# Kernel tuning notes

Hardware: AMD Instinct MI355X
Metric: run time of the kernel (lower is better)

Reference implementation:

```python
import jax, jax.numpy as jnp
import numpy as np

N = 50000          # num nodes
E = 800000         # num edges
DIM = 64           # node_channels
EDGE_DIM = 16
HEADS = 4
TIME_STEP = 3
NEG_SLOPE = 0.2
HC = HEADS * DIM


def setup_inputs() -> dict:
    key = jax.random.key(0)
    ks = jax.random.split(key, 16)
    rn = lambda k, shape, s=0.1: (jax.random.normal(k, shape, jnp.float32) * s)
    return {
        "x": jax.random.normal(ks[0], (N, DIM), jnp.float32),
        "edge_index": jax.random.randint(ks[1], (2, E), 0, N, jnp.int32),
        "edge_attr": jax.random.normal(ks[2], (E, EDGE_DIM), jnp.float32),
        "Wn": rn(ks[3], (DIM, HC)),
        "We": rn(ks[4], (EDGE_DIM, HC)),
        "Wa": rn(ks[5], (1, HEADS, 3 * DIM)),
        "Ws": rn(ks[6], (HC, DIM)),
        "b": jnp.zeros((DIM,), jnp.float32),
        "Wih": rn(ks[7], (3 * DIM, DIM)),
        "Whh": rn(ks[8], (3 * DIM, DIM)),
        "bih": rn(ks[9], (3 * DIM,)),
        "bhh": rn(ks[10], (3 * DIM,)),
        "gamma": jnp.ones((DIM,), jnp.float32),
        "beta": jnp.zeros((DIM,), jnp.float32),
    }


def _mhta(x, src, dst, edge_attr, Wn, We, Wa, Ws, b):
    xp = x @ Wn                                    # [N, H*C]
    ep = (edge_attr @ We).reshape(-1, HEADS, DIM)  # [E, H, C]
    x_j = xp[src].reshape(-1, HEADS, DIM)          # source nodes
    x_i = xp[dst].reshape(-1, HEADS, DIM)          # target nodes
    wa = Wa.reshape(HEADS, 3, DIM)                 # split of cat([x_i, e, x_j])
    alpha = (jnp.einsum('ehc,hc->eh', x_i, wa[:, 0])
             + jnp.einsum('ehc,hc->eh', ep, wa[:, 1])
             + jnp.einsum('ehc,hc->eh', x_j, wa[:, 2]))
    alpha = jax.nn.leaky_relu(alpha, NEG_SLOPE)
    # segment softmax grouped by target node (PyG softmax)
    amax = jax.ops.segment_max(alpha, dst, num_segments=N)
    alpha = jnp.exp(alpha - amax[dst])
    denom = jax.ops.segment_sum(alpha, dst, num_segments=N)
    alpha = alpha / (denom[dst] + 1e-16)
    msg = (alpha[:, :, None] * ep * x_j).reshape(-1, HC)
    aggr = jax.ops.segment_sum(msg, dst, num_segments=N)  # [N, H*C]
    return aggr @ Ws + b


def _gru_step(m, h, Wih, Whh, bih, bhh):
    gi = m @ Wih.T + bih
    gh = h @ Whh.T + bhh
    i_r, i_z, i_n = jnp.split(gi, 3, axis=-1)
    h_r, h_z, h_n = jnp.split(gh, 3, axis=-1)
    r = jax.nn.sigmoid(i_r + h_r)
    z = jax.nn.sigmoid(i_z + h_z)
    n = jnp.tanh(i_n + r * h_n)
    return (1.0 - z) * n + z * h


def _layernorm(x, gamma, beta, eps=1e-5):
    mu = jnp.mean(x, axis=-1, keepdims=True)
    var = jnp.mean((x - mu) ** 2, axis=-1, keepdims=True)
    return (x - mu) * jax.lax.rsqrt(var + eps) * gamma + beta


def reference(x, edge_index, edge_attr, Wn, We, Wa, Ws, b,
              Wih, Whh, bih, bhh, gamma, beta):
    src, dst = edge_index[0], edge_index[1]
    h = x  # h0 = x.unsqueeze(0) in torch (seq_len=1 GRU)
    xc = x
    for _ in range(TIME_STEP):
        m = jax.nn.celu(_mhta(xc, src, dst, edge_attr, Wn, We, Wa, Ws, b))
        h = _gru_step(m, h, Wih, Whh, bih, bhh)
        xc = _layernorm(h, gamma, beta)
    return xc
```

## Files before the change

### kernel.cpp

```cpp
#include <hip/hip_runtime.h>
#include <math.h>

#define NNODES 50000
#define NEDGES 800000

typedef _Float16 f16;
typedef _Float16 f16x2 __attribute__((ext_vector_type(2)));
typedef _Float16 f16x4 __attribute__((ext_vector_type(4)));
typedef _Float16 f16x8 __attribute__((ext_vector_type(8)));
typedef float f32x4 __attribute__((ext_vector_type(4)));

#define FMAMIX_LO(ACC, PV, WRD) \
    asm("v_fma_mix_f32 %0, %1, %2, %0 op_sel_hi:[0,1,0]" \
        : "+v"(ACC) : "v"(PV), "v"(WRD))
#define FMAMIX_HI(ACC, PV, WRD) \
    asm("v_fma_mix_f32 %0, %1, %2, %0 op_sel:[0,1,0] op_sel_hi:[0,1,0]" \
        : "+v"(ACC) : "v"(PV), "v"(WRD))

__device__ inline uint pk16(float a, float b) {
    union { f16x2 h; uint u; } c;
    c.h[0] = (f16)a; c.h[1] = (f16)b;
    return c.u;
}
__device__ inline f16x2 bc16(uint u) {
    union { uint u; f16x2 h; } c; c.u = u; return c.h;
}
__device__ inline float wred_max(float v) {
#pragma unroll
    for (int off = 32; off; off >>= 1) v = fmaxf(v, __shfl_xor(v, off, 64));
    return v;
}
__device__ inline float wred_sum(float v) {
#pragma unroll
    for (int off = 32; off; off >>= 1) v += __shfl_xor(v, off, 64);
    return v;
}
__device__ inline float wred_max16(float v) {
#pragma unroll
    for (int off = 8; off; off >>= 1) v = fmaxf(v, __shfl_xor(v, off, 64));
    return v;
}
__device__ inline float wred_sum16(float v) {
#pragma unroll
    for (int off = 8; off; off >>= 1) v += __shfl_xor(v, off, 64);
    return v;
}


__global__ __launch_bounds__(256) void k_fold1(
    const float* __restrict__ Wn, const float* __restrict__ We,
    const float* __restrict__ Wa,
    float* __restrict__ wnwa0, float* __restrict__ wnwa2,
    float* __restrict__ wewa1)
{
    int t = threadIdx.x;
    {
        int k = t >> 2, h = t & 3;
        float s0 = 0.f, s2 = 0.f;
        for (int c = 0; c < 64; c++) {
            float wn = Wn[k * 256 + h * 64 + c];
            s0 = fmaf(wn, Wa[h * 192 + c], s0);
            s2 = fmaf(wn, Wa[h * 192 + 128 + c], s2);
        }
        wnwa0[t] = s0;
        wnwa2[t] = s2;
    }
    if (t < 64) {
        int k = t >> 2, h = t & 3;
        float s1 = 0.f;
        for (int c = 0; c < 64; c++)
            s1 = fmaf(We[k * 256 + h * 64 + c], Wa[h * 192 + 64 + c], s1);
        wewa1[t] = s1;
    }
}

__global__ __launch_bounds__(256) void k_fold2(
    const float* __restrict__ Wn, const float* __restrict__ We,
    const float* __restrict__ Wih, const float* __restrict__ Whh,
    const float* __restrict__ Ws, const float* __restrict__ wnwa0,
    const float* __restrict__ wnwa2,
    f16* __restrict__ WeB, f16* __restrict__ WsP, f16* __restrict__ WihP,
    f16* __restrict__ WhhP, f16* __restrict__ WnB, f16* __restrict__ awB)
{
    int gid = blockIdx.x * 256 + threadIdx.x;
    const int STR = 8 * 256;
    for (int idx = gid; idx < 128; idx += STR) {
        int ks = idx >> 6, l = idx & 63;
        int lg = l >> 4, c = l & 15;
        f16* o = awB + (size_t)idx * 8;
        for (int j = 0; j < 8; j++) {
            int k = ks * 32 + lg * 8 + j;
            float v = (c < 4) ? wnwa0[k * 4 + c] : ((c < 8) ? wnwa2[k * 4 + (c - 4)] : 0.f);
            o[j] = (f16)v;
        }
    }
    for (int idx = gid; idx < 2048; idx += STR) {
        int l = idx & 63, tt = (idx >> 6) & 15, ks = idx >> 10;
        int lg = l >> 4, ll = l & 15;
        f16* o = WnB + (size_t)idx * 8;
        for (int j = 0; j < 8; j++)
            o[j] = (f16)Wn[(ks * 32 + lg * 8 + j) * 256 + tt * 16 + ll];
    }
    for (int idx = gid; idx < 1024; idx += STR) {
        int tt = idx >> 6, l = idx & 63;
        int lg = l >> 4, ll = l & 15;
        f16* o = WeB + (size_t)idx * 4;
        for (int j = 0; j < 4; j++)
            o[j] = (f16)We[(lg * 4 + j) * 256 + tt * 16 + ll];
    }
    for (int e = gid; e < 2048; e += STR) {
        int l = e & 63, tt = (e >> 6) & 3, ks = e >> 8;
        int lg = l >> 4, ll = l & 15;
        f16* o = WsP + (size_t)e * 8;
        for (int j = 0; j < 8; j++)
            o[j] = (f16)Ws[(ks * 32 + lg * 8 + j) * 64 + tt * 16 + ll];
    }
    for (int e = gid; e < 1536; e += STR) {
        int l = e & 63, q = e >> 6;
        int tt = q % 12, ks = q / 12;
        int lg = l >> 4, ll = l & 15;
        int outc = tt * 16 + ll;
        for (int j = 0; j < 8; j++) {
            int k = ks * 32 + lg * 8 + j;
            WihP[(size_t)e * 8 + j] = (f16)Wih[outc * 64 + k];
            WhhP[(size_t)e * 8 + j] = (f16)Whh[outc * 64 + k];
        }
    }
}

__global__ __launch_bounds__(256) void k_hist(const int* __restrict__ dst, int* __restrict__ counts)
{
    int e = blockIdx.x * 256 + threadIdx.x;
    atomicAdd(&counts[dst[e]], 1);
}

__global__ __launch_bounds__(1024) void k_scan(const int* __restrict__ counts,
                                               int* __restrict__ row_ptr, int n)
{
    __shared__ int wsum[16];
    int t = threadIdx.x, wid = t >> 6, lane = t & 63;
    int running = 0;
    for (int base = 0; base < n; base += 1024) {
        int idx = base + t;
        int c = (idx < n) ? counts[idx] : 0;
        int v = c;
#pragma unroll
        for (int off = 1; off < 64; off <<= 1) {
            int u = __shfl_up(v, off, 64);
            if (lane >= off) v += u;
        }
        if (lane == 63) wsum[wid] = v;
        __syncthreads();
        int wpre = 0, tot = 0;
#pragma unroll
        for (int wk = 0; wk < 16; wk++) {
            int s = wsum[wk];
            if (wk < wid) wpre += s;
            tot += s;
        }
        if (idx < n) row_ptr[idx] = running + wpre + v - c;
        running += tot;
        __syncthreads();
    }
    if (t == 0) row_ptr[n] = running;
}

__global__ __launch_bounds__(256) void k_scatter(
    const int* __restrict__ srcv, const int* __restrict__ dstv,
    const float* __restrict__ ea, const float* __restrict__ wewa1,
    const int* __restrict__ row_ptr, int* __restrict__ fill,
    int* __restrict__ csr_src, uint* __restrict__ ae16c,
    uint* __restrict__ ea16_csr)
{
    __shared__ float w[64];
    int t = threadIdx.x;
    if (t < 64) w[t] = wewa1[t];
    __syncthreads();
    int e = blockIdx.x * 256 + t;
    int d = dstv[e];
    int pos = row_ptr[d] + atomicAdd(&fill[d], 1);
    csr_src[pos] = srcv[e];
    const float4* p = (const float4*)(ea + (size_t)e * 16);
    float4 v0 = p[0], v1 = p[1], v2 = p[2], v3 = p[3];
    float eav[16] = {v0.x, v0.y, v0.z, v0.w, v1.x, v1.y, v1.z, v1.w,
                     v2.x, v2.y, v2.z, v2.w, v3.x, v3.y, v3.z, v3.w};
    float a0 = 0.f, a1 = 0.f, a2 = 0.f, a3 = 0.f;
#pragma unroll
    for (int k = 0; k < 16; k++) {
        a0 = fmaf(eav[k], w[k * 4 + 0], a0);
        a1 = fmaf(eav[k], w[k * 4 + 1], a1);
        a2 = fmaf(eav[k], w[k * 4 + 2], a2);
        a3 = fmaf(eav[k], w[k * 4 + 3], a3);
    }
    uint2 ae2; ae2.x = pk16(a0, a1); ae2.y = pk16(a2, a3);
    *(uint2*)(ae16c + (size_t)pos * 2) = ae2;
    uint4 pa, pb;
    pa.x = pk16(eav[0], eav[1]);  pa.y = pk16(eav[2], eav[3]);
    pa.z = pk16(eav[4], eav[5]);  pa.w = pk16(eav[6], eav[7]);
    pb.x = pk16(eav[8], eav[9]);  pb.y = pk16(eav[10], eav[11]);
    pb.z = pk16(eav[12], eav[13]); pb.w = pk16(eav[14], eav[15]);
    uint4* d16 = (uint4*)(ea16_csr + (size_t)pos * 8);
    d16[0] = pa; d16[1] = pb;
}


__global__ __launch_bounds__(256) void k_xpaij(
    const float* __restrict__ xc, const f16* __restrict__ WnB,
    const f16* __restrict__ awB, f16* __restrict__ xp16,
    float* __restrict__ aijI, float* __restrict__ aijJ)
{
    int t = threadIdx.x, w = t >> 6, l = t & 63;
    int lg = l >> 4, ll = l & 15;
    int wbase = blockIdx.x * 64 + w * 16;
    int nodeA = wbase + ll;
    int nA = nodeA < NNODES ? nodeA : NNODES - 1;

    f16x8 afr[2];
#pragma unroll
    for (int ks = 0; ks < 2; ks++) {
        const float* xpr = xc + (size_t)nA * 64 + ks * 32 + lg * 8;
        float4 a0 = *(const float4*)xpr;
        float4 a1 = *(const float4*)(xpr + 4);
        f16x8 v;
        v[0] = (f16)a0.x; v[1] = (f16)a0.y; v[2] = (f16)a0.z; v[3] = (f16)a0.w;
        v[4] = (f16)a1.x; v[5] = (f16)a1.y; v[6] = (f16)a1.z; v[7] = (f16)a1.w;
        afr[ks] = v;
    }
    f32x4 zero = {0.f, 0.f, 0.f, 0.f};
    f32x4 c[16];
#pragma unroll
    for (int tt = 0; tt < 16; tt++) c[tt] = zero;
    f32x4 caw = zero;
    const f16x8* WnV = (const f16x8*)WnB;
    const f16x8* awV = (const f16x8*)awB;
#pragma unroll
    for (int ks = 0; ks < 2; ks++) {
        caw = __builtin_amdgcn_mfma_f32_16x16x32_f16(afr[ks], awV[ks * 64 + l], caw, 0, 0, 0);
#pragma unroll
        for (int tt = 0; tt < 16; tt++)
            c[tt] = __builtin_amdgcn_mfma_f32_16x16x32_f16(
                afr[ks], WnV[(ks * 16 + tt) * 64 + l], c[tt], 0, 0, 0);
    }
#pragma unroll
    for (int i = 0; i < 4; i++) {
        int node = wbase + lg * 4 + i;
        if (node < NNODES) {
            f16x8 o0, o1;
#pragma unroll
            for (int tt = 0; tt < 8; tt++) o0[tt] = (f16)c[tt][i];
#pragma unroll
            for (int tt = 0; tt < 8; tt++) o1[tt] = (f16)c[8 + tt][i];
            f16* dstp = xp16 + (size_t)node * 256 + ll * 16;
            *(f16x8*)dstp = o0;
            *(f16x8*)(dstp + 8) = o1;
            if (ll < 4)      aijI[(size_t)node * 4 + ll] = caw[i];
            else if (ll < 8) aijJ[(size_t)node * 4 + (ll - 4)] = caw[i];
        }
    }
}

#define LEAKY(v) ((v) > 0.f ? (v) : 0.2f * (v))

__global__ __launch_bounds__(256) void k_node(
    const int* __restrict__ row_ptr, const int* __restrict__ csr_src,
    const uint* __restrict__ ae16c, const float* __restrict__ aijI,
    const float* __restrict__ aijJ, const f16* __restrict__ xp16,
    const uint* __restrict__ ea16_csr, const f16* __restrict__ WeB,
    f16* __restrict__ aggr16)
{
    __shared__ float wbuf[4][64][4];
    __shared__ uint  eabuf[4][64][8];
    __shared__ int   srcbuf[4][64];
    int t = threadIdx.x, wid = t >> 6, lane = t & 63;
    int ll = lane & 15, g = lane >> 4;
    int n = blockIdx.x * 4 + wid;
    uint4 z4 = {0u, 0u, 0u, 0u};
    *(uint4*)&eabuf[wid][lane][0] = z4;
    *(uint4*)&eabuf[wid][lane][4] = z4;
    f16x4 wb[16];
#pragma unroll
    for (int tt = 0; tt < 16; tt++)
        wb[tt] = *(const f16x4*)(WeB + (size_t)(tt * 64 + lane) * 4);
    int r0 = row_ptr[n], r1 = row_ptr[n + 1];
    int deg = r1 - r0;
    float acc[16];
#pragma unroll
    for (int tt = 0; tt < 16; tt++) acc[tt] = 0.f;
    f32x4 zacc = {0.f, 0.f, 0.f, 0.f};

    auto agg_chunk = [&](int c) {
        int4 s4 = *(const int4*)&srcbuf[wid][c * 16 + g * 4];
        const f16* xr0 = xp16 + ((size_t)(uint)s4.x) * 256 + ll * 16;
        const f16* xr1 = xp16 + ((size_t)(uint)s4.y) * 256 + ll * 16;
        const f16* xr2 = xp16 + ((size_t)(uint)s4.z) * 256 + ll * 16;
        const f16* xr3 = xp16 + ((size_t)(uint)s4.w) * 256 + ll * 16;
        uint4 xA[4], xB[4];
        xA[0] = *(const uint4*)xr0; xB[0] = *(const uint4*)(xr0 + 8);
        xA[1] = *(const uint4*)xr1; xB[1] = *(const uint4*)(xr1 + 8);
        xA[2] = *(const uint4*)xr2; xB[2] = *(const uint4*)(xr2 + 8);
        xA[3] = *(const uint4*)xr3; xB[3] = *(const uint4*)(xr3 + 8);
        f16x4 eaf = *(const f16x4*)((const f16*)&eabuf[wid][c * 16 + ll][0] + g * 4);
        float4 w4 = *(const float4*)&wbuf[wid][c * 16 + ll][0];
        f16 av[4] = {(f16)w4.x, (f16)w4.y, (f16)w4.z, (f16)w4.w};
        f16x4 Ah[4];
#pragma unroll
        for (int h = 0; h < 4; h++)
#pragma unroll
            for (int j = 0; j < 4; j++)
                Ah[h][j] = eaf[j] * av[h];
#pragma unroll
        for (int h = 0; h < 4; h++) {
            f32x4 p0 = __builtin_amdgcn_mfma_f32_16x16x16f16(Ah[h], wb[h * 4 + 0], zacc, 0, 0, 0);
            f32x4 p1 = __builtin_amdgcn_mfma_f32_16x16x16f16(Ah[h], wb[h * 4 + 1], zacc, 0, 0, 0);
            f32x4 p2 = __builtin_amdgcn_mfma_f32_16x16x16f16(Ah[h], wb[h * 4 + 2], zacc, 0, 0, 0);
            f32x4 p3 = __builtin_amdgcn_mfma_f32_16x16x16f16(Ah[h], wb[h * 4 + 3], zacc, 0, 0, 0);
#pragma unroll
            for (int ttl = 0; ttl < 4; ttl++) {
                int tt = h * 4 + ttl;
                f32x4 pv = ttl == 0 ? p0 : (ttl == 1 ? p1 : (ttl == 2 ? p2 : p3));
                int q = tt & 7;
#pragma unroll
                for (int r = 0; r < 4; r++) {
                    uint4 xs = (tt < 8) ? xA[r] : xB[r];
                    uint wrd = (q >> 1) == 0 ? xs.x
                             : ((q >> 1) == 1 ? xs.y : ((q >> 1) == 2 ? xs.z : xs.w));
                    float pvf = pv[r];
                    if (q & 1) FMAMIX_HI(acc[tt], pvf, wrd);
                    else       FMAMIX_LO(acc[tt], pvf, wrd);
                }
            }
        }
    };

    if (deg > 0 && deg <= 64) {
        float4 ai = *(const float4*)(aijI + (size_t)n * 4);
        float al0 = -1e30f, al1 = -1e30f, al2 = -1e30f, al3 = -1e30f;
        int sreg = 0;
        if (lane < deg) {
            int p = r0 + lane;
            sreg = csr_src[p];
            uint2 ae2 = *(const uint2*)(ae16c + (size_t)p * 2);
            f16x2 aelo = bc16(ae2.x), aehi = bc16(ae2.y);
            float4 aj = *(const float4*)(aijJ + (size_t)sreg * 4);
            const uint4* ep16 = (const uint4*)(ea16_csr + (size_t)p * 8);
            uint4 ua = ep16[0], ub = ep16[1];
            *(uint4*)&eabuf[wid][lane][0] = ua;
            *(uint4*)&eabuf[wid][lane][4] = ub;
            al0 = LEAKY(ai.x + (float)aelo[0] + aj.x);
            al1 = LEAKY(ai.y + (float)aelo[1] + aj.y);
            al2 = LEAKY(ai.z + (float)aehi[0] + aj.z);
            al3 = LEAKY(ai.w + (float)aehi[1] + aj.w);
        }
        srcbuf[wid][lane] = (lane < deg) ? sreg : 0;
        float m0, m1, m2, m3, s0, s1, s2, s3;
        float p0, p1, p2, p3;
        if (deg <= 16) {
            m0 = wred_max16(al0); m1 = wred_max16(al1);
            m2 = wred_max16(al2); m3 = wred_max16(al3);
            p0 = (lane < deg) ? __expf(al0 - m0) : 0.f;
            p1 = (lane < deg) ? __expf(al1 - m1) : 0.f;
            p2 = (lane < deg) ? __expf(al2 - m2) : 0.f;
            p3 = (lane < deg) ? __expf(al3 - m3) : 0.f;
            s0 = wred_sum16(p0); s1 = wred_sum16(p1);
            s2 = wred_sum16(p2); s3 = wred_sum16(p3);
        } else {
            m0 = wred_max(al0); m1 = wred_max(al1);
            m2 = wred_max(al2); m3 = wred_max(al3);
            p0 = (lane < deg) ? __expf(al0 - m0) : 0.f;
            p1 = (lane < deg) ? __expf(al1 - m1) : 0.f;
            p2 = (lane < deg) ? __expf(al2 - m2) : 0.f;
            p3 = (lane < deg) ? __expf(al3 - m3) : 0.f;
            s0 = wred_sum(p0); s1 = wred_sum(p1);
            s2 = wred_sum(p2); s3 = wred_sum(p3);
        }
        float4 w4v;
        w4v.x = p0 * (1.f / (s0 + 1e-16f));
        w4v.y = p1 * (1.f / (s1 + 1e-16f));
        w4v.z = p2 * (1.f / (s2 + 1e-16f));
        w4v.w = p3 * (1.f / (s3 + 1e-16f));
        *(float4*)&wbuf[wid][lane][0] = w4v;
        asm volatile("s_waitcnt lgkmcnt(0)" ::: "memory");
        int nch = (deg + 15) >> 4;
        for (int c = 0; c < nch; c++) agg_chunk(c);
    } else if (deg > 0) {
        float4 ai = *(const float4*)(aijI + (size_t)n * 4);
        float m0 = -1e30f, m1 = -1e30f, m2 = -1e30f, m3 = -1e30f;
        float s0 = 0.f, s1 = 0.f, s2 = 0.f, s3 = 0.f;
        for (int base = r0; base < r1; base += 64) {
            int p = base + lane;
            if (p < r1) {
                int s = csr_src[p];
                uint2 ae2 = *(const uint2*)(ae16c + (size_t)p * 2);
                f16x2 aelo = bc16(ae2.x), aehi = bc16(ae2.y);
                float4 aj = *(const float4*)(aijJ + (size_t)s * 4);
                float al0 = LEAKY(ai.x + (float)aelo[0] + aj.x);
                float al1 = LEAKY(ai.y + (float)aelo[1] + aj.y);
                float al2 = LEAKY(ai.z + (float)aehi[0] + aj.z);
                float al3 = LEAKY(ai.w + (float)aehi[1] + aj.w);
                float nm;
                nm = fmaxf(m0, al0); s0 = s0 * __expf(m0 - nm) + __expf(al0 - nm); m0 = nm;
                nm = fmaxf(m1, al1); s1 = s1 * __expf(m1 - nm) + __expf(al1 - nm); m1 = nm;
                nm = fmaxf(m2, al2); s2 = s2 * __expf(m2 - nm) + __expf(al2 - nm); m2 = nm;
                nm = fmaxf(m3, al3); s3 = s3 * __expf(m3 - nm) + __expf(al3 - nm); m3 = nm;
            }
        }
#pragma unroll
        for (int off = 32; off; off >>= 1) {
            float om, os, nm;
            om = __shfl_xor(m0, off, 64); os = __shfl_xor(s0, off, 64);
            nm = fmaxf(m0, om); s0 = s0 * __expf(m0 - nm) + os * __expf(om - nm); m0 = nm;
            om = __shfl_xor(m1, off, 64); os = __shfl_xor(s1, off, 64);
            nm = fmaxf(m1, om); s1 = s1 * __expf(m1 - nm) + os * __expf(om - nm); m1 = nm;
            om = __shfl_xor(m2, off, 64); os = __shfl_xor(s2, off, 64);
            nm = fmaxf(m2, om); s2 = s2 * __expf(m2 - nm) + os * __expf(om - nm); m2 = nm;
            om = __shfl_xor(m3, off, 64); os = __shfl_xor(s3, off, 64);
            nm = fmaxf(m3, om); s3 = s3 * __expf(m3 - nm) + os * __expf(om - nm); m3 = nm;
        }
        float rd0 = 1.f / (s0 + 1e-16f), rd1 = 1.f / (s1 + 1e-16f);
        float rd2 = 1.f / (s2 + 1e-16f), rd3 = 1.f / (s3 + 1e-16f);
        for (int base = r0; base < r1; base += 64) {
            int cnt = min(64, r1 - base);
            float4 w4v = {0.f, 0.f, 0.f, 0.f};
            int sreg = 0;
            if (lane < cnt) {
                int p = base + lane;
                sreg = csr_src[p];
                uint2 ae2 = *(const uint2*)(ae16c + (size_t)p * 2);
                f16x2 aelo = bc16(ae2.x), aehi = bc16(ae2.y);
                float4 aj = *(const float4*)(aijJ + (size_t)sreg * 4);
                const uint4* ep16 = (const uint4*)(ea16_csr + (size_t)p * 8);
                uint4 ua = ep16[0], ub = ep16[1];
                *(uint4*)&eabuf[wid][lane][0] = ua;
                *(uint4*)&eabuf[wid][lane][4] = ub;
                float al0 = LEAKY(ai.x + (float)aelo[0] + aj.x);
                float al1 = LEAKY(ai.y + (float)aelo[1] + aj.y);
                float al2 = LEAKY(ai.z + (float)aehi[0] + aj.z);
                float al3 = LEAKY(ai.w + (float)aehi[1] + aj.w);
                w4v.x = __expf(al0 - m0) * rd0;
                w4v.y = __expf(al1 - m1) * rd1;
                w4v.z = __expf(al2 - m2) * rd2;
                w4v.w = __expf(al3 - m3) * rd3;
            } else {
                *(uint4*)&eabuf[wid][lane][0] = z4;
                *(uint4*)&eabuf[wid][lane][4] = z4;
            }
            *(float4*)&wbuf[wid][lane][0] = w4v;
            srcbuf[wid][lane] = (lane < cnt) ? sreg : 0;
            asm volatile("s_waitcnt lgkmcnt(0)" ::: "memory");
            int nch = (cnt + 15) >> 4;
            for (int c = 0; c < nch; c++) agg_chunk(c);
            asm volatile("s_waitcnt lgkmcnt(0)" ::: "memory");
        }
    }
#pragma unroll
    for (int tt = 0; tt < 16; tt++) {
        float v = acc[tt];
        v += __shfl_xor(v, 16, 64);
        v += __shfl_xor(v, 32, 64);
        acc[tt] = v;
    }
    f16* ag = aggr16 + (size_t)n * 256;
#pragma unroll
    for (int tt = 0; tt < 16; tt++)
        if ((tt >> 2) == g) ag[tt * 16 + ll] = (f16)acc[tt];
}

__global__ __launch_bounds__(256) void k_post(
    const f16* __restrict__ aggr16, const f16* __restrict__ WsP,
    const float* __restrict__ bvec, const float* __restrict__ h_in,
    float* __restrict__ h_out, const f16* __restrict__ WihP,
    const f16* __restrict__ WhhP, const float* __restrict__ bih,
    const float* __restrict__ bhh, const float* __restrict__ gamma,
    const float* __restrict__ beta, float* __restrict__ xc_out)
{
    __shared__ __align__(16) f16 m_lds[4][16][72];
    int t = threadIdx.x, w = t >> 6, l = t & 63;
    int lg = l >> 4, ll = l & 15;
    int nb = blockIdx.x * 64 + w * 16;
    int nodeA = nb + ll;
    int nodeAc = nodeA < NNODES ? nodeA : NNODES - 1;

    f32x4 zero = {0.f, 0.f, 0.f, 0.f};
    f32x4 acc1[4];
#pragma unroll
    for (int tt = 0; tt < 4; tt++) acc1[tt] = zero;
    const f16x8* WsV = (const f16x8*)WsP;
#pragma unroll
    for (int ks = 0; ks < 8; ks++) {
        f16x8 a = *(const f16x8*)(aggr16 + (size_t)nodeAc * 256 + ks * 32 + lg * 8);
#pragma unroll
        for (int tt = 0; tt < 4; tt++) {
            f16x8 b = WsV[(ks * 4 + tt) * 64 + l];
            acc1[tt] = __builtin_amdgcn_mfma_f32_16x16x32_f16(a, b, acc1[tt], 0, 0, 0);
        }
    }
#pragma unroll
    for (int tt = 0; tt < 4; tt++) {
        float bj = bvec[tt * 16 + ll];
#pragma unroll
        for (int i = 0; i < 4; i++) {
            float v = acc1[tt][i] + bj;
            v = v > 0.f ? v : (__expf(v) - 1.f);
            m_lds[w][lg * 4 + i][tt * 16 + ll] = (f16)v;
        }
    }
    asm volatile("s_waitcnt lgkmcnt(0)" ::: "memory");

    f16x8 mf[2], hf[2];
#pragma unroll
    for (int ks = 0; ks < 2; ks++) {
        mf[ks] = *(const f16x8*)(&m_lds[w][ll][ks * 32 + lg * 8]);
        const float* hp = h_in + (size_t)nodeAc * 64 + ks * 32 + lg * 8;
        float4 h0 = *(const float4*)(hp);
        float4 h1 = *(const float4*)(hp + 4);
        f16x8 hh;
        hh[0] = (f16)h0.x; hh[1] = (f16)h0.y; hh[2] = (f16)h0.z; hh[3] = (f16)h0.w;
        hh[4] = (f16)h1.x; hh[5] = (f16)h1.y; hh[6] = (f16)h1.z; hh[7] = (f16)h1.w;
        hf[ks] = hh;
    }
    f32x4 accI[12], accH[12];
#pragma unroll
    for (int tt = 0; tt < 12; tt++) { accI[tt] = zero; accH[tt] = zero; }
    const f16x8* WiV = (const f16x8*)WihP;
    const f16x8* WhV = (const f16x8*)WhhP;
#pragma unroll
    for (int ks = 0; ks < 2; ks++) {
#pragma unroll
        for (int tt = 0; tt < 12; tt++) {
            f16x8 bi = WiV[(ks * 12 + tt) * 64 + l];
            accI[tt] = __builtin_amdgcn_mfma_f32_16x16x32_f16(mf[ks], bi, accI[tt], 0, 0, 0);
            f16x8 bh = WhV[(ks * 12 + tt) * 64 + l];
            accH[tt] = __builtin_amdgcn_mfma_f32_16x16x32_f16(hf[ks], bh, accH[tt], 0, 0, 0);
        }
    }

    float bI[12], bH[12];
#pragma unroll
    for (int tt = 0; tt < 12; tt++) {
        bI[tt] = bih[ll + 16 * tt];
        bH[tt] = bhh[ll + 16 * tt];
    }
    float ga[4], be[4];
#pragma unroll
    for (int u = 0; u < 4; u++) { ga[u] = gamma[ll + 16 * u]; be[u] = beta[ll + 16 * u]; }
    float hnew[4][4];
#pragma unroll
    for (int i = 0; i < 4; i++) {
        int node = nb + lg * 4 + i;
        int nc = node < NNODES ? node : NNODES - 1;
        const float* hrow = h_in + (size_t)nc * 64 + ll;
#pragma unroll
        for (int u = 0; u < 4; u++) {
            float hv = hrow[16 * u];
            float r = 1.f / (1.f + __expf(-(accI[u][i] + bI[u] + accH[u][i] + bH[u])));
            float z = 1.f / (1.f + __expf(-(accI[u + 4][i] + bI[u + 4] + accH[u + 4][i] + bH[u + 4])));
            float pre = accI[u + 8][i] + bI[u + 8] + r * (accH[u + 8][i] + bH[u + 8]);
            float e2 = __expf(2.f * pre);
            float nn = 1.f - 2.f / (e2 + 1.f);
            hnew[i][u] = (1.f - z) * nn + z * hv;
        }
    }
#pragma unroll
    for (int i = 0; i < 4; i++) {
        float s = hnew[i][0] + hnew[i][1] + hnew[i][2] + hnew[i][3];
        float q = hnew[i][0] * hnew[i][0] + hnew[i][1] * hnew[i][1]
                + hnew[i][2] * hnew[i][2] + hnew[i][3] * hnew[i][3];
#pragma unroll
        for (int off = 1; off < 16; off <<= 1) {
            s += __shfl_xor(s, off, 64);
            q += __shfl_xor(q, off, 64);
        }
        float mu = s * (1.f / 64.f);
        float var = q * (1.f / 64.f) - mu * mu;
        float rstd = rsqrtf(var + 1e-5f);
        int node = nb + lg * 4 + i;
        if (node < NNODES) {
            float* ho = h_out + (size_t)node * 64 + ll;
            float* xo = xc_out + (size_t)node * 64 + ll;
#pragma unroll
            for (int u = 0; u < 4; u++) {
                ho[16 * u] = hnew[i][u];
                xo[16 * u] = (hnew[i][u] - mu) * rstd * ga[u] + be[u];
            }
        }
    }
}


extern "C" void kernel_launch(void* const* d_in, const int* in_sizes, int n_in,
                              void* d_out, int out_size, void* d_ws, size_t ws_size,
                              hipStream_t stream)
{
    const float* x         = (const float*)d_in[0];
    const int*   edge_index= (const int*)d_in[1];
    const float* edge_attr = (const float*)d_in[2];
    const float* Wn        = (const float*)d_in[3];
    const float* We        = (const float*)d_in[4];
    const float* Wa        = (const float*)d_in[5];
    const float* Ws        = (const float*)d_in[6];
    const float* bv        = (const float*)d_in[7];
    const float* Wih       = (const float*)d_in[8];
    const float* Whh       = (const float*)d_in[9];
    const float* bih       = (const float*)d_in[10];
    const float* bhh       = (const float*)d_in[11];
    const float* gamma     = (const float*)d_in[12];
    const float* beta      = (const float*)d_in[13];
    float* out = (float*)d_out;

    const int* src = edge_index;
    const int* dst = edge_index + NEDGES;

    char* w = (char*)d_ws;
    auto alloc = [&](size_t bytes) {
        char* p = w;
        w += (bytes + 255) & ~(size_t)255;
        return p;
    };
    f16*   xp16     = (f16*)alloc((size_t)NNODES * 256 * 2);
    f16*   aggr16   = (f16*)alloc((size_t)NNODES * 256 * 2);
    uint*  ae16c    = (uint*)alloc((size_t)NEDGES * 2 * 4);
    uint*  ea16_csr = (uint*)alloc((size_t)NEDGES * 8 * 4);
    float* hbuf     = (float*)alloc((size_t)NNODES * 64 * 4);
    float* aijI     = (float*)alloc((size_t)NNODES * 4 * 4);
    float* aijJ     = (float*)alloc((size_t)NNODES * 4 * 4);
    int*   counts   = (int*)alloc((size_t)NNODES * 4);
    int*   fill     = (int*)alloc((size_t)NNODES * 4);
    int*   row_ptr  = (int*)alloc((size_t)(NNODES + 1) * 4);
    int*   csr_src  = (int*)alloc((size_t)NEDGES * 4);
    float* wnwa0    = (float*)alloc(256 * 4);
    float* wnwa2    = (float*)alloc(256 * 4);
    float* wewa1    = (float*)alloc(64 * 4);
    f16*   WeB      = (f16*)alloc(1024 * 4 * 2);
    f16*   WsP      = (f16*)alloc(2048 * 8 * 2);
    f16*   WihP     = (f16*)alloc(1536 * 8 * 2);
    f16*   WhhP     = (f16*)alloc(1536 * 8 * 2);
    f16*   WnB      = (f16*)alloc(2048 * 8 * 2);
    f16*   awB      = (f16*)alloc(128 * 8 * 2);

    k_fold1<<<1, 256, 0, stream>>>(Wn, We, Wa, wnwa0, wnwa2, wewa1);
    hipMemsetAsync(counts, 0, (size_t)NNODES * 4, stream);
    hipMemsetAsync(fill, 0, (size_t)NNODES * 4, stream);
    k_hist<<<NEDGES / 256, 256, 0, stream>>>(dst, counts);
    k_fold2<<<8, 256, 0, stream>>>(Wn, We, Wih, Whh, Ws, wnwa0, wnwa2,
                                   WeB, WsP, WihP, WhhP, WnB, awB);
    k_scan<<<1, 1024, 0, stream>>>(counts, row_ptr, NNODES);
    k_scatter<<<NEDGES / 256, 256, 0, stream>>>(src, dst, edge_attr, wewa1,
                                                row_ptr, fill, csr_src,
                                                ae16c, ea16_csr);

    for (int step = 0; step < 3; step++) {
        const float* xc_in = (step == 0) ? x : out;
        const float* h_in  = (step == 0) ? x : hbuf;
        k_xpaij<<<(NNODES + 63) / 64, 256, 0, stream>>>(xc_in, WnB, awB,
                                                        xp16, aijI, aijJ);
        k_node<<<NNODES / 4, 256, 0, stream>>>(row_ptr, csr_src, ae16c, aijI,
                                               aijJ, xp16, ea16_csr, WeB, aggr16);
        k_post<<<(NNODES + 63) / 64, 256, 0, stream>>>(
            aggr16, WsP, bv, h_in, hbuf, WihP, WhhP, bih, bhh, gamma, beta, out);
    }
}
```

Baseline: 575.6 us.

## Fuse next-step node projection into GRU post kernel and parallelize CSR scan

Replaces the single-block serial scan with a three-pass multi-block scan. k_hist now records each edge's atomic rank, so k_scatter no longer needs a second atomic fill pass. The k_xpaij projection for steps 1 and 2 is folded into k_post: the layernormed output goes through LDS as f16 and is multiplied by Wn and the attention weights with MFMA, which removes the intermediate xc write and read and two kernel launches. The costs are an extra per-edge rank buffer and higher register pressure in k_post.

```diff
diff --git a/kernel.cpp b/kernel.cpp
--- a/kernel.cpp
+++ b/kernel.cpp
@@ -128,47 +128,72 @@
     }
 }
 
-__global__ __launch_bounds__(256) void k_hist(const int* __restrict__ dst, int* __restrict__ counts)
+__global__ __launch_bounds__(256) void k_hist(const int* __restrict__ dst,
+                                              int* __restrict__ counts,
+                                              int* __restrict__ rankv)
 {
     int e = blockIdx.x * 256 + threadIdx.x;
-    atomicAdd(&counts[dst[e]], 1);
-}
-
-__global__ __launch_bounds__(1024) void k_scan(const int* __restrict__ counts,
-                                               int* __restrict__ row_ptr, int n)
+    rankv[e] = atomicAdd(&counts[dst[e]], 1);
+}
+
+__global__ __launch_bounds__(1024) void k_scan1(const int* __restrict__ counts,
+                                                int* __restrict__ psum)
 {
     __shared__ int wsum[16];
     int t = threadIdx.x, wid = t >> 6, lane = t & 63;
-    int running = 0;
-    for (int base = 0; base < n; base += 1024) {
-        int idx = base + t;
-        int c = (idx < n) ? counts[idx] : 0;
-        int v = c;
-#pragma unroll
-        for (int off = 1; off < 64; off <<= 1) {
-            int u = __shfl_up(v, off, 64);
-            if (lane >= off) v += u;
-        }
-        if (lane == 63) wsum[wid] = v;
-        __syncthreads();
-        int wpre = 0, tot = 0;
-#pragma unroll
-        for (int wk = 0; wk < 16; wk++) {
-            int s = wsum[wk];
-            if (wk < wid) wpre += s;
-            tot += s;
-        }
-        if (idx < n) row_ptr[idx] = running + wpre + v - c;
-        running += tot;
-        __syncthreads();
-    }
-    if (t == 0) row_ptr[n] = running;
+    int idx = blockIdx.x * 1024 + t;
+    int c = (idx < NNODES) ? counts[idx] : 0;
+    int v = c;
+#pragma unroll
+    for (int off = 32; off; off >>= 1) v += __shfl_xor(v, off, 64);
+    if (lane == 0) wsum[wid] = v;
+    __syncthreads();
+    if (t == 0) {
+        int s = 0;
+        for (int wk = 0; wk < 16; wk++) s += wsum[wk];
+        psum[blockIdx.x] = s;
+    }
+}
+
+__global__ __launch_bounds__(64) void k_scan0(int* __restrict__ psum, int nb)
+{
+    if (threadIdx.x == 0) {
+        int run = 0;
+        for (int b = 0; b < nb; b++) { int s = psum[b]; psum[b] = run; run += s; }
+    }
+}
+
+__global__ __launch_bounds__(1024) void k_scan2(const int* __restrict__ counts,
+                                                const int* __restrict__ psum,
+                                                int* __restrict__ row_ptr)
+{
+    __shared__ int wsum[16];
+    int t = threadIdx.x, wid = t >> 6, lane = t & 63;
+    int idx = blockIdx.x * 1024 + t;
+    int c = (idx < NNODES) ? counts[idx] : 0;
+    int v = c;
+#pragma unroll
+    for (int off = 1; off < 64; off <<= 1) {
+        int u = __shfl_up(v, off, 64);
+        if (lane >= off) v += u;
+    }
+    if (lane == 63) wsum[wid] = v;
+    __syncthreads();
+    int wpre = 0;
+#pragma unroll
+    for (int wk = 0; wk < 16; wk++) {
+        int s = wsum[wk];
+        if (wk < wid) wpre += s;
+    }
+    if (idx < NNODES) row_ptr[idx] = psum[blockIdx.x] + wpre + v - c;
+    if (idx == 0) row_ptr[NNODES] = NEDGES;
 }
 
 __global__ __launch_bounds__(256) void k_scatter(
     const int* __restrict__ srcv, const int* __restrict__ dstv,
+    const int* __restrict__ rankv,
     const float* __restrict__ ea, const float* __restrict__ wewa1,
-    const int* __restrict__ row_ptr, int* __restrict__ fill,
+    const int* __restrict__ row_ptr,
     int* __restrict__ csr_src, uint* __restrict__ ae16c,
     uint* __restrict__ ea16_csr)
 {
@@ -178,7 +203,7 @@
     __syncthreads();
     int e = blockIdx.x * 256 + t;
     int d = dstv[e];
-    int pos = row_ptr[d] + atomicAdd(&fill[d], 1);
+    int pos = row_ptr[d] + rankv[e];
     csr_src[pos] = srcv[e];
     const float4* p = (const float4*)(ea + (size_t)e * 16);
     float4 v0 = p[0], v1 = p[1], v2 = p[2], v3 = p[3];
@@ -471,7 +496,10 @@
     float* __restrict__ h_out, const f16* __restrict__ WihP,
     const f16* __restrict__ WhhP, const float* __restrict__ bih,
     const float* __restrict__ bhh, const float* __restrict__ gamma,
-    const float* __restrict__ beta, float* __restrict__ xc_out)
+    const float* __restrict__ beta, const f16* __restrict__ WnB,
+    const f16* __restrict__ awB, f16* __restrict__ xp16,
+    float* __restrict__ aijI, float* __restrict__ aijJ,
+    float* __restrict__ xc_out, int last)
 {
     __shared__ __align__(16) f16 m_lds[4][16][72];
     int t = threadIdx.x, w = t >> 6, l = t & 63;
@@ -574,14 +602,54 @@
         float var = q * (1.f / 64.f) - mu * mu;
         float rstd = rsqrtf(var + 1e-5f);
         int node = nb + lg * 4 + i;
+        bool ok = node < NNODES;
+        float* ho = h_out + (size_t)node * 64 + ll;
+        float* xo = xc_out + (size_t)node * 64 + ll;
+#pragma unroll
+        for (int u = 0; u < 4; u++) {
+            float xcv = (hnew[i][u] - mu) * rstd * ga[u] + be[u];
+            if (ok) {
+                ho[16 * u] = hnew[i][u];
+                if (last) xo[16 * u] = xcv;
+            }
+            m_lds[w][lg * 4 + i][16 * u + ll] = (f16)xcv;
+        }
+    }
+    if (last) return;
+    asm volatile("s_waitcnt lgkmcnt(0)" ::: "memory");
+
+    f16x8 afr[2];
+#pragma unroll
+    for (int ks = 0; ks < 2; ks++)
+        afr[ks] = *(const f16x8*)(&m_lds[w][ll][ks * 32 + lg * 8]);
+    f32x4 c[16];
+#pragma unroll
+    for (int tt = 0; tt < 16; tt++) c[tt] = zero;
+    f32x4 caw = zero;
+    const f16x8* WnV = (const f16x8*)WnB;
+    const f16x8* awV = (const f16x8*)awB;
+#pragma unroll
+    for (int ks = 0; ks < 2; ks++) {
+        caw = __builtin_amdgcn_mfma_f32_16x16x32_f16(afr[ks], awV[ks * 64 + l], caw, 0, 0, 0);
+#pragma unroll
+        for (int tt = 0; tt < 16; tt++)
+            c[tt] = __builtin_amdgcn_mfma_f32_16x16x32_f16(
+                afr[ks], WnV[(ks * 16 + tt) * 64 + l], c[tt], 0, 0, 0);
+    }
+#pragma unroll
+    for (int i = 0; i < 4; i++) {
+        int node = nb + lg * 4 + i;
         if (node < NNODES) {
-            float* ho = h_out + (size_t)node * 64 + ll;
-            float* xo = xc_out + (size_t)node * 64 + ll;
-#pragma unroll
-            for (int u = 0; u < 4; u++) {
-                ho[16 * u] = hnew[i][u];
-                xo[16 * u] = (hnew[i][u] - mu) * rstd * ga[u] + be[u];
-            }
+            f16x8 o0, o1;
+#pragma unroll
+            for (int tt = 0; tt < 8; tt++) o0[tt] = (f16)c[tt][i];
+#pragma unroll
+            for (int tt = 0; tt < 8; tt++) o1[tt] = (f16)c[8 + tt][i];
+            f16* dstp = xp16 + (size_t)node * 256 + ll * 16;
+            *(f16x8*)dstp = o0;
+            *(f16x8*)(dstp + 8) = o1;
+            if (ll < 4)      aijI[(size_t)node * 4 + ll] = caw[i];
+            else if (ll < 8) aijJ[(size_t)node * 4 + (ll - 4)] = caw[i];
         }
     }
 }
@@ -624,9 +692,10 @@
     float* aijI     = (float*)alloc((size_t)NNODES * 4 * 4);
     float* aijJ     = (float*)alloc((size_t)NNODES * 4 * 4);
     int*   counts   = (int*)alloc((size_t)NNODES * 4);
-    int*   fill     = (int*)alloc((size_t)NNODES * 4);
+    int*   rankv    = (int*)alloc((size_t)NEDGES * 4);
     int*   row_ptr  = (int*)alloc((size_t)(NNODES + 1) * 4);
     int*   csr_src  = (int*)alloc((size_t)NEDGES * 4);
+    int*   psum     = (int*)alloc(64 * 4);
     float* wnwa0    = (float*)alloc(256 * 4);
     float* wnwa2    = (float*)alloc(256 * 4);
     float* wewa1    = (float*)alloc(64 * 4);
@@ -637,25 +706,28 @@
     f16*   WnB      = (f16*)alloc(2048 * 8 * 2);
     f16*   awB      = (f16*)alloc(128 * 8 * 2);
 
+    const int NSCAN = (NNODES + 1023) / 1024;
+
     k_fold1<<<1, 256, 0, stream>>>(Wn, We, Wa, wnwa0, wnwa2, wewa1);
     hipMemsetAsync(counts, 0, (size_t)NNODES * 4, stream);
-    hipMemsetAsync(fill, 0, (size_t)NNODES * 4, stream);
-    k_hist<<<NEDGES / 256, 256, 0, stream>>>(dst, counts);
+    k_hist<<<NEDGES / 256, 256, 0, stream>>>(dst, counts, rankv);
     k_fold2<<<8, 256, 0, stream>>>(Wn, We, Wih, Whh, Ws, wnwa0, wnwa2,
                                    WeB, WsP, WihP, WhhP, WnB, awB);
-    k_scan<<<1, 1024, 0, stream>>>(counts, row_ptr, NNODES);
-    k_scatter<<<NEDGES / 256, 256, 0, stream>>>(src, dst, edge_attr, wewa1,
-                                                row_ptr, fill, csr_src,
+    k_scan1<<<NSCAN, 1024, 0, stream>>>(counts, psum);
+    k_scan0<<<1, 64, 0, stream>>>(psum, NSCAN);
+    k_scan2<<<NSCAN, 1024, 0, stream>>>(counts, psum, row_ptr);
+    k_scatter<<<NEDGES / 256, 256, 0, stream>>>(src, dst, rankv, edge_attr,
+                                                wewa1, row_ptr, csr_src,
                                                 ae16c, ea16_csr);
 
+    k_xpaij<<<(NNODES + 63) / 64, 256, 0, stream>>>(x, WnB, awB,
+                                                    xp16, aijI, aijJ);
     for (int step = 0; step < 3; step++) {
-        const float* xc_in = (step == 0) ? x : out;
-        const float* h_in  = (step == 0) ? x : hbuf;
-        k_xpaij<<<(NNODES + 63) / 64, 256, 0, stream>>>(xc_in, WnB, awB,
-                                                        xp16, aijI, aijJ);
+        const float* h_in = (step == 0) ? x : hbuf;
         k_node<<<NNODES / 4, 256, 0, stream>>>(row_ptr, csr_src, ae16c, aijI,
                                                aijJ, xp16, ea16_csr, WeB, aggr16);
         k_post<<<(NNODES + 63) / 64, 256, 0, stream>>>(
-            aggr16, WsP, bv, h_in, hbuf, WihP, WhhP, bih, bhh, gamma, beta, out);
-    }
-}
+            aggr16, WsP, bv, h_in, hbuf, WihP, WhhP, bih, bhh, gamma, beta,
+            WnB, awB, xp16, aijI, aijJ, out, step == 2 ? 1 : 0);
+    }
+}
```

Measured after the change: 525.1 us. 8.8% less time.
